# Performance work log

Hardware: AMD Instinct MI355X
Metric: run time of the kernel (lower is better)

## Reference

```python
import jax, jax.numpy as jnp
import numpy as np
from math import sqrt

B, IN_C, OUT_C, H, W, WDIM, K = 16, 512, 512, 64, 64, 512, 3
EPS = 1e-8
LRELU_SLOPE = 0.2


def setup_inputs() -> dict:
    key = jax.random.key(0)
    ks = jax.random.split(key, 5)
    return {
        "x": jax.random.normal(ks[0], (B, IN_C, H, W), dtype=jnp.float32),
        "w": jax.random.normal(ks[1], (B, WDIM), dtype=jnp.float32),
        "noise": jax.random.normal(ks[2], (B, 1, H, W), dtype=jnp.float32),
        "linear_w": jax.random.normal(ks[3], (IN_C, WDIM), dtype=jnp.float32),
        "linear_b": jnp.ones((IN_C,), dtype=jnp.float32),
        "conv_w": jax.random.normal(ks[4], (OUT_C, IN_C, K, K), dtype=jnp.float32),
        "scale_noise": jnp.zeros((OUT_C,), dtype=jnp.float32),
        "bias": jnp.zeros((OUT_C,), dtype=jnp.float32),
    }


def reference(x, w, noise, linear_w, linear_b, conv_w, scale_noise, bias):
    # EqualizerStraights: equalized-lr linear, scale = 1/sqrt(w_dim)
    s = w @ (linear_w * (1.0 / sqrt(WDIM))).T + linear_b  # [b, in_c]
    # Weight_Demod: equalized conv weight, scale = 1/sqrt(in_c*k*k)
    base_w = conv_w * (1.0 / sqrt(IN_C * K * K))  # [out, in, k, k]
    weights = base_w[None] * s[:, None, :, None, None]  # [b, out, in, k, k]
    sigma_inv = jax.lax.rsqrt(
        jnp.sum(weights * weights, axis=(2, 3, 4), keepdims=True) + EPS)
    weights = weights * sigma_inv

    def conv1(xi, wi):  # xi [in,h,w], wi [out,in,k,k]
        return jax.lax.conv_general_dilated(
            xi[None], wi, window_strides=(1, 1), padding="SAME",
            dimension_numbers=("NCHW", "OIHW", "NCHW"))[0]

    y = jax.vmap(conv1)(x, weights)  # [b, out, h, w]
    y = y + scale_noise[None, :, None, None] * noise
    return jax.nn.leaky_relu(y + bias[None, :, None, None], negative_slope=LRELU_SLOPE)
```

## Files before the change

kernel.cpp:

```cpp
#include <hip/hip_runtime.h>
#include <hip/hip_bf16.h>
#include <stdint.h>

typedef __bf16 bf16_t;
typedef __bf16 bf16x8 __attribute__((ext_vector_type(8)));
typedef short short8 __attribute__((ext_vector_type(8)));
typedef float f32x4 __attribute__((ext_vector_type(4)));

#define RS512  0.044194173824159216f
#define RS4608 0.014731391274719739f

__global__ void k_style(const float* __restrict__ w, const float* __restrict__ lw,
                        const float* __restrict__ lb, float* __restrict__ s) {
  int b = blockIdx.y;
  int c = blockIdx.x * 256 + threadIdx.x;
  const float4* wr = (const float4*)(w + b * 512);
  const float4* lr = (const float4*)(lw + (size_t)c * 512);
  float acc = 0.f;
#pragma unroll 4
  for (int d = 0; d < 128; ++d) {
    float4 a = wr[d], q = lr[d];
    acc += a.x * q.x + a.y * q.y + a.z * q.z + a.w * q.w;
  }
  s[b * 512 + c] = acc * RS512 + lb[c];
}

__global__ void k_wprep(const float* __restrict__ cw, float* __restrict__ wsq,
                        bf16_t* __restrict__ bwf, f32x4* __restrict__ zb) {
  if (blockIdx.x == 0) zb[threadIdx.x] = (f32x4)0.f;
  int idx = blockIdx.x * 256 + threadIdx.x;
  int o = idx >> 9, i = idx & 511;
  float v[9];
  float ss = 0.f;
#pragma unroll
  for (int t = 0; t < 9; ++t) {
    float x = cw[(size_t)idx * 9 + t] * RS4608;
    v[t] = x;
    ss += x * x;
  }
  wsq[idx] = ss;
  int lane = (o & 15) | (((i >> 3) & 3) << 4);
  int base_blk = (i >> 5) * 32 + (o >> 4);
#pragma unroll
  for (int t = 0; t < 9; ++t) {
    size_t e = ((size_t)(t * 512 + base_blk) << 9) + lane * 8 + (i & 7);
    bwf[e] = (bf16_t)v[t];
  }
}

__global__ void k_sigma(const float* __restrict__ s, const float* __restrict__ wsq,
                        float* __restrict__ sinv) {
  __shared__ float s2[512];
  int b = blockIdx.y;
  int o = blockIdx.x * 256 + threadIdx.x;
  for (int i = threadIdx.x; i < 512; i += 256) {
    float v = s[b * 512 + i];
    s2[i] = v * v;
  }
  __syncthreads();
  const float4* qr = (const float4*)(wsq + (size_t)o * 512);
  float acc = 0.f;
#pragma unroll 4
  for (int d = 0; d < 128; ++d) {
    float4 q = qr[d];
    acc += q.x * s2[4 * d] + q.y * s2[4 * d + 1] + q.z * s2[4 * d + 2] + q.w * s2[4 * d + 3];
  }
  sinv[b * 512 + o] = rsqrtf(acc + 1e-8f);
}

__global__ void k_xt(const float* __restrict__ x, const float* __restrict__ s,
                     bf16_t* __restrict__ xt) {
  int ic = blockIdx.x, h = blockIdx.y, b = blockIdx.z;
  __shared__ __align__(16) bf16_t tile[8192];
  int t = threadIdx.x;
  int wcol = t & 63;
  int g = t >> 6;
#pragma unroll
  for (int blk = 0; blk < 4; ++blk) {
    int grp = blk * 4 + g;
    bf16x8 vec;
#pragma unroll
    for (int k = 0; k < 8; ++k) {
      int i = ic * 128 + grp * 8 + k;
      float v = x[(((size_t)b * 512 + i) * 64 + h) * 64 + wcol] * s[b * 512 + i];
      vec[k] = (bf16_t)v;
    }
    int chunk = grp ^ (wcol & 15);
    *(bf16x8*)((char*)tile + wcol * 256 + chunk * 16) = vec;
  }
  __syncthreads();
#pragma unroll
  for (int j = 0; j < 4; ++j) {
    int flat = j * 256 + t;
    int wo = flat >> 4, ig8 = flat & 15;
    int chunk = ig8 ^ (wo & 15);
    bf16x8 v = *(bf16x8*)((char*)tile + wo * 256 + chunk * 16);
    int cc = ic * 4 + (ig8 >> 2);
    int kgr = ig8 & 3;
    size_t dst = ((((size_t)b * 64 + h) * 16 + cc) << 11) + (kgr << 9) + (size_t)wo * 8;
    *(bf16x8*)(xt + dst) = v;
  }
}

#define AS1 __attribute__((address_space(1)))
#define AS3 __attribute__((address_space(3)))

__device__ __forceinline__ void gl16(const void* g, void* l) {
  __builtin_amdgcn_global_load_lds((const AS1 void*)g, (AS3 void*)l, 16, 0, 0);
}

#define XT0 4096u

__global__ __launch_bounds__(512, 4) void k_conv(
    const char* __restrict__ wsb,
    const bf16_t* __restrict__ bwf,
    const float* __restrict__ sinv, const float* __restrict__ noise,
    const float* __restrict__ snz, const float* __restrict__ bias,
    float* __restrict__ out) {
  __shared__ __align__(16) char lds[50176];

  const int t = threadIdx.x;
  const int rq = blockIdx.x;
  const int OY = blockIdx.y;
  const int b = blockIdx.z;
  const int h0 = rq * 4;
  const int lane = t & 63;
  const int wv = t >> 6;
  const int wm = wv & 1;
  const int wn = wv >> 1;

  f32x4 acc[4][4] = {};
  bf16x8 wA[4], wB[4];

  uint32_t xsoff[3], xdst[3], xsel[3];
#pragma unroll
  for (int k = 0; k < 3; ++k) {
    int slot = wv * 3 + k, row = slot >> 2, q = slot & 3;
    int gr = h0 - 1 + row;
    int valid = ((unsigned)gr < 64u) ? 1 : 0;
    uint32_t so = valid ? (XT0 + (uint32_t)b * 4194304u + (uint32_t)gr * 65536u +
                           (uint32_t)q * 1024u)
                        : 0u;
    xsoff[k] = __builtin_amdgcn_readfirstlane(so);
    xdst[k] = __builtin_amdgcn_readfirstlane((uint32_t)(1024 + row * 4096 + q * 1024));
    xsel[k] = __builtin_amdgcn_readfirstlane((uint32_t)valid);
  }

  auto stX = [&](int k, uint32_t cxoff, int xb) {
    uint32_t co = xsel[k] ? cxoff : 0u;
    gl16(wsb + xsoff[k] + co + (size_t)(lane * 16), lds + xdst[k] + (uint32_t)(xb * 24576));
  };

  const size_t wbase0 = ((size_t)(OY * 8 + wm * 4)) << 10;
  auto loadW = [&](int tap, int c, bf16x8* d) {
    const char* p = (const char*)bwf + wbase0 + (((size_t)(tap * 16 + c)) << 15);
#pragma unroll
    for (int mi = 0; mi < 4; ++mi)
      d[mi] = *(const bf16x8*)(p + mi * 1024 + (size_t)(lane * 16));
  };

  const uint32_t pXbase =
      (uint32_t)(1024 + wn * 4096 + (lane >> 4) * 1024 + (lane & 15) * 16);
  const bool c0 = (lane & 15) == 0;
  const bool c15 = (lane & 15) == 15;

#define CTAP(J, XB, AF)                                                        \
  {                                                                            \
    const int ky = (J) / 3, kx = (J) % 3;                                      \
    __builtin_amdgcn_s_setprio(1);                                             \
    _Pragma("unroll") for (int col = 0; col < 4; ++col) {                      \
      short8 xv = *(const short8*)(lds + pXbase +                              \
                                   (uint32_t)((XB) * 24576 + ky * 4096 +       \
                                              col * 256 + (kx - 1) * 16));     \
      if (kx == 0 && col == 0) xv = c0 ? (short8)0 : xv;                       \
      if (kx == 2 && col == 3) xv = c15 ? (short8)0 : xv;                      \
      bf16x8 bv = __builtin_bit_cast(bf16x8, xv);                              \
      _Pragma("unroll") for (int mi = 0; mi < 4; ++mi)                         \
          acc[mi][col] = __builtin_amdgcn_mfma_f32_16x16x32_bf16(              \
              AF[mi], bv, acc[mi][col], 0, 0, 0);                              \
    }                                                                          \
    __builtin_amdgcn_s_setprio(0);                                             \
  }

#define CHUNK(C, XB, P, LAST)                                                  \
  {                                                                            \
    _Pragma("unroll") for (int j = 0; j < 9; ++j) {                            \
      if (!(LAST) && j < 3) stX(j, (uint32_t)(((C) + 1) * 4096), (XB) ^ 1);    \
      if (j < 8) {                                                             \
        if (((j + (P)) & 1) == 0) loadW(j + 1, (C), wB);                       \
        else loadW(j + 1, (C), wA);                                            \
      } else if (!(LAST)) {                                                    \
        if (((j + (P)) & 1) == 0) loadW(0, (C) + 1, wB);                       \
        else loadW(0, (C) + 1, wA);                                            \
      }                                                                        \
      if (((j + (P)) & 1) == 0) CTAP(j, (XB), wA)                              \
      else CTAP(j, (XB), wB)                                                   \
    }                                                                          \
    __syncthreads();                                                           \
  }

#pragma unroll
  for (int k = 0; k < 3; ++k) stX(k, 0u, 0);
  loadW(0, 0, wA);
  __syncthreads();

#pragma unroll 1
  for (int ci = 0; ci < 7; ++ci) {
    const int c = ci * 2;
    CHUNK(c, 0, 0, 0);
    CHUNK(c + 1, 1, 1, 0);
  }
  CHUNK(14, 0, 0, 0);
  CHUNK(15, 1, 1, 1);

  const float* sb = sinv + b * 512;
  const int og = OY * 128 + wm * 64 + ((lane >> 4) << 2);
  const int colb = lane & 15;
  const int prow = h0 + wn;
  float nzv[4];
#pragma unroll
  for (int col = 0; col < 4; ++col)
    nzv[col] = noise[(size_t)b * 4096 + prow * 64 + col * 16 + colb];
#pragma unroll
  for (int mi = 0; mi < 4; ++mi) {
#pragma unroll
    for (int r = 0; r < 4; ++r) {
      int o = og + mi * 16 + r;
      float sv = sb[o];
      float nw = snz[o];
      float bv = bias[o];
      float* orow = out + (((size_t)b * 512 + o) * 64 + prow) * 64;
#pragma unroll
      for (int col = 0; col < 4; ++col) {
        float v = acc[mi][col][r] * sv + nw * nzv[col] + bv;
        orow[col * 16 + colb] = v > 0.f ? v : 0.2f * v;
      }
    }
  }
}

extern "C" void kernel_launch(void* const* d_in, const int* in_sizes, int n_in,
                              void* d_out, int out_size, void* d_ws, size_t ws_size,
                              hipStream_t stream) {
  const float* x     = (const float*)d_in[0];
  const float* w     = (const float*)d_in[1];
  const float* noise = (const float*)d_in[2];
  const float* lw    = (const float*)d_in[3];
  const float* lb    = (const float*)d_in[4];
  const float* cw    = (const float*)d_in[5];
  const float* snz   = (const float*)d_in[6];
  const float* bias  = (const float*)d_in[7];
  float* out = (float*)d_out;

  char* ws = (char*)d_ws;
  char*   zbuf = ws;
  bf16_t* xt   = (bf16_t*)(ws + 4096);
  bf16_t* bwf  = (bf16_t*)(ws + 67112960);
  float*  s    = (float*)(ws + 71831552);
  float*  sinv = (float*)(ws + 71864320);
  float*  wsq  = (float*)(ws + 71897088);

  k_style<<<dim3(2, 16), 256, 0, stream>>>(w, lw, lb, s);
  k_wprep<<<dim3(1024), 256, 0, stream>>>(cw, wsq, bwf, (f32x4*)zbuf);
  k_sigma<<<dim3(2, 16), 256, 0, stream>>>(s, wsq, sinv);
  k_xt<<<dim3(4, 64, 16), 256, 0, stream>>>(x, s, xt);
  k_conv<<<dim3(16, 4, 16), 512, 0, stream>>>(ws, bwf, sinv, noise, snz, bias, out);
}
```

Before: 312.3 us.

## Switch conv to 32x32x16 MFMA tiles with matching weight/activation layouts

Replaces the 16x16x32 bf16 MFMA tiling of the implicit-GEMM conv with 32x32x16 MFMAs, which means fewer instructions and larger per-instruction tiles. The packed weight layout, the activation transpose layout and the LDS read pattern are reworked to feed the new operand shapes. The epilogue is remapped to the 32x32 accumulator layout. The per-chunk __syncthreads is replaced by an explicit vmcnt wait plus a raw barrier, and the barrier is skipped on the last chunk. The swizzle in the transpose kernel is removed, which risks LDS bank conflicts, and the partial vmcnt wait relies on a precise count of outstanding loads.

```diff
diff --git a/kernel.cpp b/kernel.cpp
--- a/kernel.cpp
+++ b/kernel.cpp
@@ -6,6 +6,7 @@
 typedef __bf16 bf16x8 __attribute__((ext_vector_type(8)));
 typedef short short8 __attribute__((ext_vector_type(8)));
 typedef float f32x4 __attribute__((ext_vector_type(4)));
+typedef float f32x16 __attribute__((ext_vector_type(16)));
 
 #define RS512  0.044194173824159216f
 #define RS4608 0.014731391274719739f
@@ -39,11 +40,11 @@
     ss += x * x;
   }
   wsq[idx] = ss;
-  int lane = (o & 15) | (((i >> 3) & 3) << 4);
-  int base_blk = (i >> 5) * 32 + (o >> 4);
+  int c32 = i >> 5, fo = o >> 5, ks = (i >> 4) & 1;
+  int ln = (o & 31) + ((i >> 3) & 1) * 32;
 #pragma unroll
   for (int t = 0; t < 9; ++t) {
-    size_t e = ((size_t)(t * 512 + base_blk) << 9) + lane * 8 + (i & 7);
+    size_t e = ((size_t)(((t * 16 + c32) * 16 + fo) * 2 + ks) << 9) + ln * 8 + (i & 7);
     bwf[e] = (bf16_t)v[t];
   }
 }
@@ -85,20 +86,14 @@
       float v = x[(((size_t)b * 512 + i) * 64 + h) * 64 + wcol] * s[b * 512 + i];
       vec[k] = (bf16_t)v;
     }
-    int chunk = grp ^ (wcol & 15);
-    *(bf16x8*)((char*)tile + wcol * 256 + chunk * 16) = vec;
+    *(bf16x8*)((char*)tile + grp * 1024 + wcol * 16) = vec;
   }
   __syncthreads();
+  char* dst = (char*)xt + ((((size_t)b * 64 + h) * 16 + ic * 4) << 12) + g * 1024 + wcol * 16;
 #pragma unroll
   for (int j = 0; j < 4; ++j) {
-    int flat = j * 256 + t;
-    int wo = flat >> 4, ig8 = flat & 15;
-    int chunk = ig8 ^ (wo & 15);
-    bf16x8 v = *(bf16x8*)((char*)tile + wo * 256 + chunk * 16);
-    int cc = ic * 4 + (ig8 >> 2);
-    int kgr = ig8 & 3;
-    size_t dst = ((((size_t)b * 64 + h) * 16 + cc) << 11) + (kgr << 9) + (size_t)wo * 8;
-    *(bf16x8*)(xt + dst) = v;
+    bf16x8 v = *(bf16x8*)((char*)tile + (j * 4 + g) * 1024 + wcol * 16);
+    *(bf16x8*)(dst + j * 4096) = v;
   }
 }
 
@@ -108,6 +103,8 @@
 __device__ __forceinline__ void gl16(const void* g, void* l) {
   __builtin_amdgcn_global_load_lds((const AS1 void*)g, (AS3 void*)l, 16, 0, 0);
 }
+
+#define VMCNT(n) asm volatile("s_waitcnt vmcnt(" #n ")" ::: "memory")
 
 #define XT0 4096u
 
@@ -117,7 +114,7 @@
     const float* __restrict__ sinv, const float* __restrict__ noise,
     const float* __restrict__ snz, const float* __restrict__ bias,
     float* __restrict__ out) {
-  __shared__ __align__(16) char lds[50176];
+  __shared__ __align__(16) char lds[51200];
 
   const int t = threadIdx.x;
   const int rq = blockIdx.x;
@@ -129,7 +126,7 @@
   const int wm = wv & 1;
   const int wn = wv >> 1;
 
-  f32x4 acc[4][4] = {};
+  f32x16 acc[2][2] = {};
   bf16x8 wA[4], wB[4];
 
   uint32_t xsoff[3], xdst[3], xsel[3];
@@ -151,33 +148,49 @@
     gl16(wsb + xsoff[k] + co + (size_t)(lane * 16), lds + xdst[k] + (uint32_t)(xb * 24576));
   };
 
-  const size_t wbase0 = ((size_t)(OY * 8 + wm * 4)) << 10;
+  const size_t wbase0 = ((size_t)(OY * 4 + wm * 2)) << 11;
   auto loadW = [&](int tap, int c, bf16x8* d) {
-    const char* p = (const char*)bwf + wbase0 + (((size_t)(tap * 16 + c)) << 15);
-#pragma unroll
-    for (int mi = 0; mi < 4; ++mi)
-      d[mi] = *(const bf16x8*)(p + mi * 1024 + (size_t)(lane * 16));
+    const char* p = (const char*)bwf + wbase0 + (((size_t)(tap * 16 + c)) << 15) +
+                    (size_t)(lane * 16);
+#pragma unroll
+    for (int f = 0; f < 2; ++f)
+#pragma unroll
+      for (int ks = 0; ks < 2; ++ks)
+        d[f * 2 + ks] = *(const bf16x8*)(p + f * 2048 + ks * 1024);
   };
 
   const uint32_t pXbase =
-      (uint32_t)(1024 + wn * 4096 + (lane >> 4) * 1024 + (lane & 15) * 16);
-  const bool c0 = (lane & 15) == 0;
-  const bool c15 = (lane & 15) == 15;
+      (uint32_t)(1024 + wn * 4096 + (lane >> 5) * 1024 + (lane & 31) * 16);
+  const bool cl = (lane & 31) == 0;
+  const bool cr = (lane & 31) == 31;
 
 #define CTAP(J, XB, AF)                                                        \
   {                                                                            \
     const int ky = (J) / 3, kx = (J) % 3;                                      \
     __builtin_amdgcn_s_setprio(1);                                             \
-    _Pragma("unroll") for (int col = 0; col < 4; ++col) {                      \
-      short8 xv = *(const short8*)(lds + pXbase +                              \
-                                   (uint32_t)((XB) * 24576 + ky * 4096 +       \
-                                              col * 256 + (kx - 1) * 16));     \
-      if (kx == 0 && col == 0) xv = c0 ? (short8)0 : xv;                       \
-      if (kx == 2 && col == 3) xv = c15 ? (short8)0 : xv;                      \
-      bf16x8 bv = __builtin_bit_cast(bf16x8, xv);                              \
-      _Pragma("unroll") for (int mi = 0; mi < 4; ++mi)                         \
-          acc[mi][col] = __builtin_amdgcn_mfma_f32_16x16x32_bf16(              \
-              AF[mi], bv, acc[mi][col], 0, 0, 0);                              \
+    _Pragma("unroll") for (int nf = 0; nf < 2; ++nf) {                         \
+      bf16x8 b0, b1;                                                           \
+      {                                                                        \
+        short8 xv = *(const short8*)(lds + pXbase +                            \
+            (uint32_t)((XB) * 24576 + ky * 4096 + nf * 512 + (kx - 1) * 16));  \
+        if (kx == 0 && nf == 0) xv = cl ? (short8)0 : xv;                      \
+        if (kx == 2 && nf == 1) xv = cr ? (short8)0 : xv;                      \
+        b0 = __builtin_bit_cast(bf16x8, xv);                                   \
+      }                                                                        \
+      {                                                                        \
+        short8 xv = *(const short8*)(lds + pXbase +                            \
+            (uint32_t)((XB) * 24576 + ky * 4096 + 2048 + nf * 512 +            \
+                       (kx - 1) * 16));                                        \
+        if (kx == 0 && nf == 0) xv = cl ? (short8)0 : xv;                      \
+        if (kx == 2 && nf == 1) xv = cr ? (short8)0 : xv;                      \
+        b1 = __builtin_bit_cast(bf16x8, xv);                                   \
+      }                                                                        \
+      _Pragma("unroll") for (int f = 0; f < 2; ++f) {                          \
+        acc[f][nf] = __builtin_amdgcn_mfma_f32_32x32x16_bf16(                  \
+            AF[f * 2 + 0], b0, acc[f][nf], 0, 0, 0);                           \
+        acc[f][nf] = __builtin_amdgcn_mfma_f32_32x32x16_bf16(                  \
+            AF[f * 2 + 1], b1, acc[f][nf], 0, 0, 0);                           \
+      }                                                                        \
     }                                                                          \
     __builtin_amdgcn_s_setprio(0);                                             \
   }
@@ -196,7 +209,7 @@
       if (((j + (P)) & 1) == 0) CTAP(j, (XB), wA)                              \
       else CTAP(j, (XB), wB)                                                   \
     }                                                                          \
-    __syncthreads();                                                           \
+    if (!(LAST)) { VMCNT(4); __builtin_amdgcn_s_barrier(); }                   \
   }
 
 #pragma unroll
@@ -214,27 +227,24 @@
   CHUNK(15, 1, 1, 1);
 
   const float* sb = sinv + b * 512;
-  const int og = OY * 128 + wm * 64 + ((lane >> 4) << 2);
-  const int colb = lane & 15;
+  const int colb = lane & 31;
+  const int rq4 = (lane >> 5) * 4;
   const int prow = h0 + wn;
-  float nzv[4];
-#pragma unroll
-  for (int col = 0; col < 4; ++col)
-    nzv[col] = noise[(size_t)b * 4096 + prow * 64 + col * 16 + colb];
-#pragma unroll
-  for (int mi = 0; mi < 4; ++mi) {
-#pragma unroll
-    for (int r = 0; r < 4; ++r) {
-      int o = og + mi * 16 + r;
+  float nz0 = noise[(size_t)b * 4096 + prow * 64 + colb];
+  float nz1 = noise[(size_t)b * 4096 + prow * 64 + 32 + colb];
+#pragma unroll
+  for (int f = 0; f < 2; ++f) {
+#pragma unroll
+    for (int r = 0; r < 16; ++r) {
+      int o = OY * 128 + wm * 64 + f * 32 + (r & 3) + 8 * (r >> 2) + rq4;
       float sv = sb[o];
       float nw = snz[o];
       float bv = bias[o];
       float* orow = out + (((size_t)b * 512 + o) * 64 + prow) * 64;
-#pragma unroll
-      for (int col = 0; col < 4; ++col) {
-        float v = acc[mi][col][r] * sv + nw * nzv[col] + bv;
-        orow[col * 16 + colb] = v > 0.f ? v : 0.2f * v;
-      }
+      float v0 = acc[f][0][r] * sv + nw * nz0 + bv;
+      float v1 = acc[f][1][r] * sv + nw * nz1 + bv;
+      orow[colb] = v0 > 0.f ? v0 : 0.2f * v0;
+      orow[32 + colb] = v1 > 0.f ? v1 : 0.2f * v1;
     }
   }
 }
```

Result: slower. 360.5 us (+15.5%).
